# Optimization experiments

Measured on AMD Instinct MI355X. Metric: run time of the kernel, lower is better.

## Reference

```python
import jax, jax.numpy as jnp
import numpy as np


def setup_inputs() -> dict:
    key = jax.random.key(0)
    ks = jax.random.split(key, 8)
    T, S, W, O = 50000, 168, 336, 48
    N = T - W - O + 1
    x = jax.random.uniform(ks[0], (T,), minval=0.5, maxval=1.5, dtype=jnp.float32)
    noise = jax.random.normal(ks[1], (N, W), dtype=jnp.float32) * 0.001  # Normal(0, std=0.001)
    level_sc = jax.random.uniform(ks[2], (), minval=-1.0, maxval=1.0, dtype=jnp.float32)
    seas_sc = jax.random.uniform(ks[3], (), minval=-1.0, maxval=1.0, dtype=jnp.float32)
    init_seas = jax.random.uniform(ks[4], (S,), minval=0.65, maxval=1.35, dtype=jnp.float32)
    W1 = jax.random.normal(ks[5], (W, W), dtype=jnp.float32) / np.float32(np.sqrt(W))
    b1 = jnp.zeros((W,), jnp.float32)
    W2 = jax.random.normal(ks[6], (W, O), dtype=jnp.float32) / np.float32(np.sqrt(W))
    b2 = jnp.zeros((O,), jnp.float32)
    return {"x": x, "noise": noise, "level_sc": level_sc, "seas_sc": seas_sc,
            "init_seas": init_seas, "W1": W1, "b1": b1, "W2": W2, "b2": b2,
            "window_size": W, "out_size": O, "lvp": 1}


def reference(x, noise, level_sc, seas_sc, init_seas, W1, b1, W2, b2,
              window_size, out_size, lvp):
    T = x.shape[0]
    a = jax.nn.sigmoid(level_sc)      # level smoothing coeff
    g = jax.nn.sigmoid(seas_sc)       # seasonal smoothing coeff
    s0 = jnp.exp(init_seas)           # [S] initial multiplicative seasonals
    # seasonals list in torch: seas[0..S-1]=s0, seas[S]=s0[0], seas[S+i]=w_i.
    # Ring buffer holds seas[i..i+S-1] at step i (starting i=1): [s0[1:], s0[0]].
    buf0 = jnp.concatenate([s0[1:], s0[:1]])
    level0 = x[0] / s0[0]

    def step(carry, xi):
        level, buf = carry
        seas_i = buf[0]
        new_level = a * xi / seas_i + (1.0 - a) * level
        new_w = g * xi / new_level + (1.0 - g) * seas_i
        new_buf = jnp.concatenate([buf[1:], new_w[None]])
        return (new_level, new_buf), (new_level, new_w, jnp.log(new_level / level))

    _, (lvls, ws, logdiffs) = jax.lax.scan(step, (level0, buf0), x[1:])
    levels = jnp.concatenate([level0[None], lvls])        # [T]
    seas_full = jnp.concatenate([s0, s0[:1], ws])         # [S+T]

    d = logdiffs[1:] - logdiffs[:-1]
    level_var_loss = jnp.mean(d * d) * lvp

    N = T - window_size - out_size + 1
    idx_in = jnp.arange(N)[:, None] + jnp.arange(window_size)[None, :]   # [N,W]
    idx_lab = jnp.arange(N)[:, None] + window_size + jnp.arange(out_size)[None, :]  # [N,O]
    lev = levels[jnp.arange(N) + window_size][:, None]    # [N,1]
    inp = jnp.log(x[idx_in] / (lev * seas_full[idx_in])) + noise   # noisy squashed inputs
    labels = jnp.log(x[idx_lab] / (lev * seas_full[idx_lab]))

    h = jnp.tanh(inp @ W1 + b1)        # tanh_no_lstm: Linear(336,336)+tanh
    out = h @ W2 + b2                  # linear_no_lstm: Linear(336,48)
    return out, labels, level_var_loss
```

## Files before the change

kernel.cpp:

```cpp
#include <hip/hip_runtime.h>
#include <hip/hip_bf16.h>

typedef __attribute__((ext_vector_type(8))) short  s16x8;
typedef __attribute__((ext_vector_type(4))) short  s16x4;
typedef __attribute__((ext_vector_type(4))) float  f32x4;

#define T_LEN 50000
#define S_LEN 168
#define W_IN  336
#define O_OUT 48
#define N_ROWS (T_LEN - W_IN - O_OUT + 1)
#define N_PAD  49664
#define NBLK   (N_PAD / 64)

__device__ inline short f2bf(float f) {
    union { float f; unsigned u; } v; v.f = f;
    unsigned u = v.u;
    unsigned r = u + 0x7fffu + ((u >> 16) & 1u);
    return (short)(r >> 16);
}

__device__ inline int bfpk(float lo, float hi) {
    float2 f2; f2.x = lo; f2.y = hi;
    __hip_bfloat162 h = __float22bfloat162_rn(f2);
    int r; __builtin_memcpy(&r, &h, 4);
    return r;
}

__device__ inline float readlane_f(float v, int l) {
    return __int_as_float(__builtin_amdgcn_readlane(__float_as_int(v), l));
}

__device__ inline float fast_tanh(float v) {
    float e = __expf(2.f * v);
    return 1.f - 2.f * __builtin_amdgcn_rcpf(e + 1.f);
}

__global__ void k_preconvert(const float* __restrict__ W1, const float* __restrict__ W2,
                             short* __restrict__ W1T, short* __restrict__ W2T,
                             float* __restrict__ S1) {
    int idx = blockIdx.x * 256 + threadIdx.x;
    const int n1 = 352 * 352;
    const int n2 = n1 + 48 * 360;
    if (idx < n1) {
        int j = idx / 352, k = idx % 352;
        W1T[idx] = (j < 336 && k < 336) ? f2bf(W1[k * 336 + j]) : (short)0;
    } else if (idx < n2) {
        int i2 = idx - n1;
        int o = i2 / 360, k = i2 % 360;
        W2T[i2] = (k < 336) ? f2bf(W2[k * 48 + o]) : (short)0;
    } else if (idx < n2 + 352) {
        int j = idx - n2;
        float s = 0.f;
        if (j < 336)
            for (int k = 0; k < 336; ++k) s += W1[k * 336 + j];
        S1[j] = s;
    }
}

#define DPP_FMA(q_, CTRL, W, RM) { \
    int t_ = __builtin_amdgcn_update_dpp(0, __float_as_int(q_), (CTRL), (RM), 0xf, true); \
    q_ = fmaf((W), __int_as_float(t_), q_); }

__global__ void k_scan(const float* __restrict__ x, const float* __restrict__ level_sc,
                       const float* __restrict__ seas_sc, const float* __restrict__ init_seas,
                       float* __restrict__ lw, float* __restrict__ seasinit) {
    __shared__ float ring[256];
    int lane = threadIdx.x;
    float a = 1.f / (1.f + expf(-level_sc[0]));
    float g = 1.f / (1.f + expf(-seas_sc[0]));
    float om = 1.f - a, omg = 1.f - g;

    for (int t = lane; t < 256; t += 64) {
        float s = 1.f;
        if (t <= S_LEN) { s = expf(init_seas[t < S_LEN ? t : 0]); seasinit[t] = s; }
        ring[t] = s;
    }
    float lpv = x[0] / expf(init_seas[0]);
    if (lane == 0) { lw[0] = lpv; lw[1] = 1.f; }
    __syncthreads();

    float om1 = om, om2v = om1 * om1, om4 = om2v * om2v, om8 = om4 * om4;
    float pl    = powf(om, (float)(lane + 1));
    float fpre  = powf(om, (float)((lane & 15) + 1));
    float fpre2 = powf(om, (float)((lane & 31) + 1));

#define SCAN(QOUT, XV, RSV) { \
    float q_ = a * (XV) * (RSV); \
    DPP_FMA(q_, 0x111, om1,  0xf); \
    DPP_FMA(q_, 0x112, om2v, 0xf); \
    DPP_FMA(q_, 0x114, om4,  0xf); \
    DPP_FMA(q_, 0x118, om8,  0xf); \
    DPP_FMA(q_, 0x142, fpre,  0xa); \
    DPP_FMA(q_, 0x143, fpre2, 0xc); \
    QOUT = q_; }

#define XLOAD(I) float xr##I = x[1 + 64 * I + lane];
    XLOAD(0) XLOAD(1) XLOAD(2) XLOAD(3) XLOAD(4) XLOAD(5) XLOAD(6) XLOAD(7)
    XLOAD(8) XLOAD(9) XLOAD(10) XLOAD(11) XLOAD(12) XLOAD(13) XLOAD(14) XLOAD(15)
#undef XLOAD

    float sA0 = ring[1 + lane];
    float Qcur; SCAN(Qcur, xr0, __builtin_amdgcn_rcpf(sA0));
    float sW = sA0;
    float ldsA = ring[65 + lane];
    float ldsB;
    int ib = 1;

#define BODY(R, RN, LIN, LOUT, CLAMP) { \
    float lvl = fmaf(pl, lpv, Qcur); \
    lpv = readlane_f(lvl, 63); \
    float w_ = fmaf(omg, sW, (g * xr##R) * __builtin_amdgcn_rcpf(lvl)); \
    float2 pk_; pk_.x = lvl; pk_.y = w_; \
    *(float2*)&lw[2 * (ib + lane)] = pk_; \
    ring[(ib + S_LEN + lane) & 255] = w_; \
    LOUT = ring[(ib + 128 + lane) & 255]; \
    float Qn_; SCAN(Qn_, xr##RN, __builtin_amdgcn_rcpf(LIN)); \
    int pidx = ib + 1024 + lane; \
    if (CLAMP) pidx = pidx > (T_LEN - 1) ? (T_LEN - 1) : pidx; \
    xr##R = x[pidx]; \
    Qcur = Qn_; sW = LIN; \
    ib += 64; }

    for (int kb = 0; kb < 47; ++kb) {
        BODY(0,1,  ldsA, ldsB, 0) BODY(1,2,  ldsB, ldsA, 0) BODY(2,3,  ldsA, ldsB, 0) BODY(3,4,  ldsB, ldsA, 0)
        BODY(4,5,  ldsA, ldsB, 0) BODY(5,6,  ldsB, ldsA, 0) BODY(6,7,  ldsA, ldsB, 0) BODY(7,8,  ldsB, ldsA, 0)
        BODY(8,9,  ldsA, ldsB, 0) BODY(9,10, ldsB, ldsA, 0) BODY(10,11,ldsA, ldsB, 0) BODY(11,12,ldsB, ldsA, 0)
        BODY(12,13,ldsA, ldsB, 0) BODY(13,14,ldsB, ldsA, 0) BODY(14,15,ldsA, ldsB, 0) BODY(15,0, ldsB, ldsA, 0)
    }
    BODY(0,1,  ldsA, ldsB, 0) BODY(1,2,  ldsB, ldsA, 0) BODY(2,3,  ldsA, ldsB, 0) BODY(3,4,  ldsB, ldsA, 0)
    BODY(4,5,  ldsA, ldsB, 0) BODY(5,6,  ldsB, ldsA, 0) BODY(6,7,  ldsA, ldsB, 0) BODY(7,8,  ldsB, ldsA, 0)
    BODY(8,9,  ldsA, ldsB, 0) BODY(9,10, ldsB, ldsA, 0) BODY(10,11,ldsA, ldsB, 0) BODY(11,12,ldsB, ldsA, 0)
    BODY(12,13,ldsA, ldsB, 0)
    BODY(13,14,ldsB, ldsA, 1) BODY(14,15,ldsA, ldsB, 1) BODY(15,0, ldsB, ldsA, 1)
    BODY(0,1,  ldsA, ldsB, 1) BODY(1,2,  ldsB, ldsA, 1) BODY(2,3,  ldsA, ldsB, 1) BODY(3,4,  ldsB, ldsA, 1)
    BODY(4,5,  ldsA, ldsB, 1) BODY(5,6,  ldsB, ldsA, 1) BODY(6,7,  ldsA, ldsB, 1) BODY(7,8,  ldsB, ldsA, 1)
    BODY(8,9,  ldsA, ldsB, 1) BODY(9,10, ldsB, ldsA, 1) BODY(10,11,ldsA, ldsB, 1) BODY(11,12,ldsB, ldsA, 1)
#undef BODY

    {
        float lvl = fmaf(pl, lpv, Qcur);
        lpv = readlane_f(lvl, 63);
        float w_ = fmaf(omg, sW, (g * xr12) * __builtin_amdgcn_rcpf(lvl));
        float2 pk_; pk_.x = lvl; pk_.y = w_;
        *(float2*)&lw[2 * (49921 + lane)] = pk_;
    }
    {
        float Qn_; SCAN(Qn_, xr13, __builtin_amdgcn_rcpf(ldsA));
        float lvl = fmaf(pl, lpv, Qn_);
        if (lane < 15) {
            float w_ = fmaf(omg, ldsA, (g * xr13) * __builtin_amdgcn_rcpf(lvl));
            float2 pk_; pk_.x = lvl; pk_.y = w_;
            *(float2*)&lw[2 * (49985 + lane)] = pk_;
        }
    }
#undef SCAN
}

__global__ void k_logs(const float* __restrict__ x, const float* __restrict__ lw,
                       const float* __restrict__ seasinit,
                       float* __restrict__ F, float* __restrict__ llev,
                       float* __restrict__ partials) {
    __shared__ float sm[258];
    __shared__ float red[256];
    int tid = threadIdx.x;
    int t = blockIdx.x * 256 + tid;
    float ll = 0.f;
    if (t < T_LEN) {
        float2 cur = *(const float2*)&lw[2 * t];
        int ps = t - S_LEN; if (ps < 0) ps = 0;
        float sv = (t <= S_LEN) ? seasinit[t] : lw[2 * ps + 1];
        F[t]  = __logf(x[t]) - __logf(sv);
        ll    = __logf(cur.x);
        llev[t] = ll;
    }
    sm[tid] = ll;
    if (tid < 2) {
        int te = blockIdx.x * 256 + 256 + tid;
        sm[256 + tid] = (te < T_LEN) ? __logf(lw[2 * te]) : 0.f;
    }
    __syncthreads();
    float s = 0.f;
    if (t < T_LEN - 2) {
        float d = sm[tid + 2] - 2.f * sm[tid + 1] + sm[tid];
        s = d * d;
    }
    red[tid] = s; __syncthreads();
    for (int off = 128; off > 0; off >>= 1) {
        if (tid < off) red[tid] += red[tid + off];
        __syncthreads();
    }
    if (tid == 0) partials[blockIdx.x] = red[0];
}

__global__ __launch_bounds__(256, 3) void k_gemm(
        const float* __restrict__ noise, const float* __restrict__ F,
        const float* __restrict__ llev, const short* __restrict__ W1T,
        const float* __restrict__ b1, const short* __restrict__ W2T,
        const float* __restrict__ b2, const float* __restrict__ S1,
        const float* __restrict__ partials, const int* __restrict__ lvp,
        float* __restrict__ out, float* __restrict__ labels, float* __restrict__ loss) {
    __shared__ __align__(16) short hlds[64][360];
    __shared__ __align__(16) float Flds[448];
    __shared__ __align__(16) float Llds[64];
    __shared__ __align__(16) float b1lds[352];
    __shared__ __align__(16) float S1lds[352];

    int t = threadIdx.x, w = t >> 6, l = t & 63;
    int lm = l & 15, lq = l >> 4;
    long n0 = (long)blockIdx.x * 64;

    if (blockIdx.x == 0 && w == 3) {
        float s = partials[l] + partials[l + 64] + partials[l + 128];
        if (l < 4) s += partials[l + 192];
#pragma unroll
        for (int off = 32; off > 0; off >>= 1) s += __shfl_down(s, off, 64);
        if (l == 0) loss[0] = s / (float)(T_LEN - 2) * (float)lvp[0];
    }

    if (t < 112)      *(f32x4*)&Flds[t * 4] = *(const f32x4*)&F[n0 + t * 4];
    else if (t < 128) *(f32x4*)&Llds[(t - 112) * 4] = *(const f32x4*)&llev[n0 + W_IN + (t - 112) * 4];
    else if (t < 216) {
        int i4 = (t - 128) * 4;
        f32x4 v = (f32x4){0.f, 0.f, 0.f, 0.f};
        if (i4 < W_IN) v = *(const f32x4*)&b1[i4];
        *(f32x4*)&b1lds[i4] = v;
    } else if (t < 304 - 48) {
        int i4 = (t - 216) * 4;
        *(f32x4*)&S1lds[i4] = *(const f32x4*)&S1[i4];
    }
    if (t < 48) *(f32x4*)&S1lds[160 + t * 4] = *(const f32x4*)&S1[160 + t * 4];

    int rbase = (w >> 1) * 32;
    int jbase = (w & 1) * 176;
    long an0 = n0 + rbase + lm;      if (an0 > N_ROWS - 2) an0 = N_ROWS - 2;
    long an1 = n0 + rbase + 16 + lm; if (an1 > N_ROWS - 2) an1 = N_ROWS - 2;
    const float* nr0 = noise + an0 * W_IN + lq * 8;
    const float* nr1 = noise + an1 * W_IN + lq * 8;

    f32x4 nc00 = *(const f32x4*)&nr0[0], nc01 = *(const f32x4*)&nr0[4];
    f32x4 nc10 = *(const f32x4*)&nr1[0], nc11 = *(const f32x4*)&nr1[4];

    f32x4 acc0[11], acc1[11];
#pragma unroll
    for (int c = 0; c < 11; ++c) { acc0[c] = (f32x4){0,0,0,0}; acc1[c] = (f32x4){0,0,0,0}; }

    __syncthreads();

    const short* w1row = &W1T[(jbase + lm) * 352 + lq * 8];
#define LDW(CT, KS) (*(const s16x8*)&w1row[(CT) * 5632 + (KS) * 32])
#define MM2(CT, AF) \
    acc0[CT] = __builtin_amdgcn_mfma_f32_16x16x32_bf16(AF, bf0, acc0[CT], 0, 0, 0); \
    acc1[CT] = __builtin_amdgcn_mfma_f32_16x16x32_bf16(AF, bf1, acc1[CT], 0, 0, 0);

#define KSTEP(KS) { \
    s16x8 bf0, bf1; \
    { int fb = rbase + lm + (KS) * 32 + lq * 8; \
      int* b0i = (int*)&bf0; int* b1i = (int*)&bf1; \
      b0i[0] = bfpk(Flds[fb+0]  + nc00[0], Flds[fb+1]  + nc00[1]); \
      b0i[1] = bfpk(Flds[fb+2]  + nc00[2], Flds[fb+3]  + nc00[3]); \
      b0i[2] = bfpk(Flds[fb+4]  + nc01[0], Flds[fb+5]  + nc01[1]); \
      b0i[3] = bfpk(Flds[fb+6]  + nc01[2], Flds[fb+7]  + nc01[3]); \
      b1i[0] = bfpk(Flds[fb+16] + nc10[0], Flds[fb+17] + nc10[1]); \
      b1i[1] = bfpk(Flds[fb+18] + nc10[2], Flds[fb+19] + nc10[3]); \
      b1i[2] = bfpk(Flds[fb+20] + nc11[0], Flds[fb+21] + nc11[1]); \
      b1i[3] = bfpk(Flds[fb+22] + nc11[2], Flds[fb+23] + nc11[3]); } \
    if ((KS) < 10) { \
      nc00 = *(const f32x4*)&nr0[((KS)+1)*32]; nc01 = *(const f32x4*)&nr0[((KS)+1)*32+4]; \
      nc10 = *(const f32x4*)&nr1[((KS)+1)*32]; nc11 = *(const f32x4*)&nr1[((KS)+1)*32+4]; \
    } \
    s16x8 af0 = LDW(0,KS), af1 = LDW(1,KS), af2 = LDW(2,KS); \
    MM2(0, af0)  af0 = LDW(3,KS); \
    MM2(1, af1)  af1 = LDW(4,KS); \
    MM2(2, af2)  af2 = LDW(5,KS); \
    MM2(3, af0)  af0 = LDW(6,KS); \
    MM2(4, af1)  af1 = LDW(7,KS); \
    MM2(5, af2)  af2 = LDW(8,KS); \
    MM2(6, af0)  af0 = LDW(9,KS); \
    MM2(7, af1)  af1 = LDW(10,KS); \
    MM2(8, af2) \
    MM2(9, af0) \
    MM2(10, af1) \
}

    KSTEP(0) KSTEP(1) KSTEP(2) KSTEP(3) KSTEP(4) KSTEP(5)
    KSTEP(6) KSTEP(7) KSTEP(8) KSTEP(9) KSTEP(10)
#undef KSTEP
#undef MM2
#undef LDW

    float lv0 = Llds[rbase + lm], lv1 = Llds[rbase + 16 + lm];
#pragma unroll
    for (int ct = 0; ct < 11; ++ct) {
        f32x4 b1q = *(f32x4*)&b1lds[jbase + ct * 16 + lq * 4];
        f32x4 s1q = *(f32x4*)&S1lds[jbase + ct * 16 + lq * 4];
        int2 p0, p1;
        p0.x = bfpk(fast_tanh(fmaf(-lv0, s1q[0], acc0[ct][0] + b1q[0])),
                    fast_tanh(fmaf(-lv0, s1q[1], acc0[ct][1] + b1q[1])));
        p0.y = bfpk(fast_tanh(fmaf(-lv0, s1q[2], acc0[ct][2] + b1q[2])),
                    fast_tanh(fmaf(-lv0, s1q[3], acc0[ct][3] + b1q[3])));
        p1.x = bfpk(fast_tanh(fmaf(-lv1, s1q[0], acc1[ct][0] + b1q[0])),
                    fast_tanh(fmaf(-lv1, s1q[1], acc1[ct][1] + b1q[1])));
        p1.y = bfpk(fast_tanh(fmaf(-lv1, s1q[2], acc1[ct][2] + b1q[2])),
                    fast_tanh(fmaf(-lv1, s1q[3], acc1[ct][3] + b1q[3])));
        *(int2*)&hlds[rbase + lm][jbase + ct * 16 + lq * 4]      = p0;
        *(int2*)&hlds[rbase + 16 + lm][jbase + ct * 16 + lq * 4] = p1;
    }
    __syncthreads();

    f32x4 a2[3];
    a2[0] = (f32x4){0,0,0,0}; a2[1] = (f32x4){0,0,0,0}; a2[2] = (f32x4){0,0,0,0};
#pragma unroll
    for (int ks = 0; ks < 11; ++ks) {
        s16x8 hf = *(s16x8*)&hlds[w * 16 + lm][ks * 32 + lq * 8];
#pragma unroll
        for (int ct = 0; ct < 3; ++ct) {
            s16x8 bf2 = *(const s16x8*)&W2T[(ct * 16 + lm) * 360 + ks * 32 + lq * 8];
            a2[ct] = __builtin_amdgcn_mfma_f32_16x16x32_bf16(hf, bf2, a2[ct], 0, 0, 0);
        }
    }

    int rloc = w * 16 + lq * 4;
#pragma unroll
    for (int ct = 0; ct < 3; ++ct) {
        float b2v = b2[ct * 16 + lm];
#pragma unroll
        for (int r = 0; r < 4; ++r) {
            long row = n0 + rloc + r;
            if (row < N_ROWS) {
                int col = ct * 16 + lm;
                out[row * O_OUT + col]    = a2[ct][r] + b2v;
                labels[row * O_OUT + col] = Flds[rloc + r + W_IN + col] - Llds[rloc + r];
            }
        }
    }
}

extern "C" void kernel_launch(void* const* d_in, const int* in_sizes, int n_in,
                              void* d_out, int out_size, void* d_ws, size_t ws_size,
                              hipStream_t stream) {
    const float* x         = (const float*)d_in[0];
    const float* noise     = (const float*)d_in[1];
    const float* level_sc  = (const float*)d_in[2];
    const float* seas_sc   = (const float*)d_in[3];
    const float* init_seas = (const float*)d_in[4];
    const float* W1        = (const float*)d_in[5];
    const float* b1        = (const float*)d_in[6];
    const float* W2        = (const float*)d_in[7];
    const float* b2        = (const float*)d_in[8];
    const int*   lvp       = (const int*)d_in[11];

    float* out    = (float*)d_out;
    float* labels = out + (long)N_ROWS * O_OUT;
    float* loss   = labels + (long)N_ROWS * O_OUT;

    float* wsf      = (float*)d_ws;
    float* lw       = wsf;
    float* seasinit = wsf + 100096;
    float* F        = wsf + 100288;
    float* llev     = wsf + 150464;
    float* partials = wsf + 200512;
    float* S1f      = wsf + 200768;
    short* W1T      = (short*)(wsf + 201152);
    short* W2T      = W1T + 352 * 352;

    k_preconvert<<<554, 256, 0, stream>>>(W1, W2, W1T, W2T, S1f);
    k_scan<<<1, 64, 0, stream>>>(x, level_sc, seas_sc, init_seas, lw, seasinit);
    k_logs<<<196, 256, 0, stream>>>(x, lw, seasinit, F, llev, partials);
    k_gemm<<<NBLK, 256, 0, stream>>>(noise, F, llev, W1T, b1, W2T, b2, S1f,
                                     partials, lvp, out, labels, loss);
}
```

Measured before the change: 157.6 us.

## Split gemm block into eight waves with one row-tile each and offload labels

The first GEMM now runs on 512 threads per block: eight waves each own 16 rows instead of four waves owning 32, halving accumulator registers per wave and using double-buffered noise prefetch. In the second phase, waves 0-3 compute the output GEMM while waves 4-7 write labels in parallel. The aim is more waves in flight to hide latency and a shorter serial epilogue. In exchange, each W1 fragment loaded now feeds one MFMA instead of two, so W1 load traffic per MFMA doubles.

Result: slower. 175.2 us, median of 2 (+11.2%).

```diff
diff --git a/kernel.cpp b/kernel.cpp
--- a/kernel.cpp
+++ b/kernel.cpp
@@ -193,7 +193,7 @@
     if (tid == 0) partials[blockIdx.x] = red[0];
 }
 
-__global__ __launch_bounds__(256, 3) void k_gemm(
+__global__ __launch_bounds__(512, 2) void k_gemm(
         const float* __restrict__ noise, const float* __restrict__ F,
         const float* __restrict__ llev, const short* __restrict__ W1T,
         const float* __restrict__ b1, const short* __restrict__ W2T,
@@ -210,7 +210,7 @@
     int lm = l & 15, lq = l >> 4;
     long n0 = (long)blockIdx.x * 64;
 
-    if (blockIdx.x == 0 && w == 3) {
+    if (blockIdx.x == 0 && w == 7) {
         float s = partials[l] + partials[l + 64] + partials[l + 128];
         if (l < 4) s += partials[l + 192];
 #pragma unroll
@@ -225,113 +225,108 @@
         f32x4 v = (f32x4){0.f, 0.f, 0.f, 0.f};
         if (i4 < W_IN) v = *(const f32x4*)&b1[i4];
         *(f32x4*)&b1lds[i4] = v;
-    } else if (t < 304 - 48) {
+    } else if (t < 304) {
         int i4 = (t - 216) * 4;
         *(f32x4*)&S1lds[i4] = *(const f32x4*)&S1[i4];
     }
-    if (t < 48) *(f32x4*)&S1lds[160 + t * 4] = *(const f32x4*)&S1[160 + t * 4];
-
-    int rbase = (w >> 1) * 32;
+
+    int rbase = (w >> 1) * 16;
     int jbase = (w & 1) * 176;
-    long an0 = n0 + rbase + lm;      if (an0 > N_ROWS - 2) an0 = N_ROWS - 2;
-    long an1 = n0 + rbase + 16 + lm; if (an1 > N_ROWS - 2) an1 = N_ROWS - 2;
+    long an0 = n0 + rbase + lm; if (an0 > N_ROWS - 2) an0 = N_ROWS - 2;
     const float* nr0 = noise + an0 * W_IN + lq * 8;
-    const float* nr1 = noise + an1 * W_IN + lq * 8;
-
-    f32x4 nc00 = *(const f32x4*)&nr0[0], nc01 = *(const f32x4*)&nr0[4];
-    f32x4 nc10 = *(const f32x4*)&nr1[0], nc11 = *(const f32x4*)&nr1[4];
-
-    f32x4 acc0[11], acc1[11];
-#pragma unroll
-    for (int c = 0; c < 11; ++c) { acc0[c] = (f32x4){0,0,0,0}; acc1[c] = (f32x4){0,0,0,0}; }
+
+    f32x4 ncE0 = *(const f32x4*)&nr0[0],  ncE1 = *(const f32x4*)&nr0[4];
+    f32x4 ncO0 = *(const f32x4*)&nr0[32], ncO1 = *(const f32x4*)&nr0[36];
+
+    f32x4 acc[11];
+#pragma unroll
+    for (int c = 0; c < 11; ++c) acc[c] = (f32x4){0.f, 0.f, 0.f, 0.f};
 
     __syncthreads();
 
     const short* w1row = &W1T[(jbase + lm) * 352 + lq * 8];
 #define LDW(CT, KS) (*(const s16x8*)&w1row[(CT) * 5632 + (KS) * 32])
-#define MM2(CT, AF) \
-    acc0[CT] = __builtin_amdgcn_mfma_f32_16x16x32_bf16(AF, bf0, acc0[CT], 0, 0, 0); \
-    acc1[CT] = __builtin_amdgcn_mfma_f32_16x16x32_bf16(AF, bf1, acc1[CT], 0, 0, 0);
-
-#define KSTEP(KS) { \
-    s16x8 bf0, bf1; \
+#define MM(CT, AF) acc[CT] = __builtin_amdgcn_mfma_f32_16x16x32_bf16(AF, bf0, acc[CT], 0, 0, 0);
+
+#define KSTEP(KS, NC0, NC1) { \
+    s16x8 bf0; \
     { int fb = rbase + lm + (KS) * 32 + lq * 8; \
-      int* b0i = (int*)&bf0; int* b1i = (int*)&bf1; \
-      b0i[0] = bfpk(Flds[fb+0]  + nc00[0], Flds[fb+1]  + nc00[1]); \
-      b0i[1] = bfpk(Flds[fb+2]  + nc00[2], Flds[fb+3]  + nc00[3]); \
-      b0i[2] = bfpk(Flds[fb+4]  + nc01[0], Flds[fb+5]  + nc01[1]); \
-      b0i[3] = bfpk(Flds[fb+6]  + nc01[2], Flds[fb+7]  + nc01[3]); \
-      b1i[0] = bfpk(Flds[fb+16] + nc10[0], Flds[fb+17] + nc10[1]); \
-      b1i[1] = bfpk(Flds[fb+18] + nc10[2], Flds[fb+19] + nc10[3]); \
-      b1i[2] = bfpk(Flds[fb+20] + nc11[0], Flds[fb+21] + nc11[1]); \
-      b1i[3] = bfpk(Flds[fb+22] + nc11[2], Flds[fb+23] + nc11[3]); } \
-    if ((KS) < 10) { \
-      nc00 = *(const f32x4*)&nr0[((KS)+1)*32]; nc01 = *(const f32x4*)&nr0[((KS)+1)*32+4]; \
-      nc10 = *(const f32x4*)&nr1[((KS)+1)*32]; nc11 = *(const f32x4*)&nr1[((KS)+1)*32+4]; \
+      int* b0i = (int*)&bf0; \
+      b0i[0] = bfpk(Flds[fb+0] + NC0[0], Flds[fb+1] + NC0[1]); \
+      b0i[1] = bfpk(Flds[fb+2] + NC0[2], Flds[fb+3] + NC0[3]); \
+      b0i[2] = bfpk(Flds[fb+4] + NC1[0], Flds[fb+5] + NC1[1]); \
+      b0i[3] = bfpk(Flds[fb+6] + NC1[2], Flds[fb+7] + NC1[3]); } \
+    if ((KS) + 2 <= 10) { \
+      NC0 = *(const f32x4*)&nr0[((KS)+2)*32]; \
+      NC1 = *(const f32x4*)&nr0[((KS)+2)*32+4]; \
     } \
     s16x8 af0 = LDW(0,KS), af1 = LDW(1,KS), af2 = LDW(2,KS); \
-    MM2(0, af0)  af0 = LDW(3,KS); \
-    MM2(1, af1)  af1 = LDW(4,KS); \
-    MM2(2, af2)  af2 = LDW(5,KS); \
-    MM2(3, af0)  af0 = LDW(6,KS); \
-    MM2(4, af1)  af1 = LDW(7,KS); \
-    MM2(5, af2)  af2 = LDW(8,KS); \
-    MM2(6, af0)  af0 = LDW(9,KS); \
-    MM2(7, af1)  af1 = LDW(10,KS); \
-    MM2(8, af2) \
-    MM2(9, af0) \
-    MM2(10, af1) \
-}
-
-    KSTEP(0) KSTEP(1) KSTEP(2) KSTEP(3) KSTEP(4) KSTEP(5)
-    KSTEP(6) KSTEP(7) KSTEP(8) KSTEP(9) KSTEP(10)
+    MM(0, af0)  af0 = LDW(3,KS); \
+    MM(1, af1)  af1 = LDW(4,KS); \
+    MM(2, af2)  af2 = LDW(5,KS); \
+    MM(3, af0)  af0 = LDW(6,KS); \
+    MM(4, af1)  af1 = LDW(7,KS); \
+    MM(5, af2)  af2 = LDW(8,KS); \
+    MM(6, af0)  af0 = LDW(9,KS); \
+    MM(7, af1)  af1 = LDW(10,KS); \
+    MM(8, af2) \
+    MM(9, af0) \
+    MM(10, af1) \
+}
+
+    KSTEP(0, ncE0, ncE1) KSTEP(1, ncO0, ncO1) KSTEP(2, ncE0, ncE1) KSTEP(3, ncO0, ncO1)
+    KSTEP(4, ncE0, ncE1) KSTEP(5, ncO0, ncO1) KSTEP(6, ncE0, ncE1) KSTEP(7, ncO0, ncO1)
+    KSTEP(8, ncE0, ncE1) KSTEP(9, ncO0, ncO1) KSTEP(10, ncE0, ncE1)
 #undef KSTEP
-#undef MM2
+#undef MM
 #undef LDW
 
-    float lv0 = Llds[rbase + lm], lv1 = Llds[rbase + 16 + lm];
+    float lv0 = Llds[rbase + lm];
 #pragma unroll
     for (int ct = 0; ct < 11; ++ct) {
         f32x4 b1q = *(f32x4*)&b1lds[jbase + ct * 16 + lq * 4];
         f32x4 s1q = *(f32x4*)&S1lds[jbase + ct * 16 + lq * 4];
-        int2 p0, p1;
-        p0.x = bfpk(fast_tanh(fmaf(-lv0, s1q[0], acc0[ct][0] + b1q[0])),
-                    fast_tanh(fmaf(-lv0, s1q[1], acc0[ct][1] + b1q[1])));
-        p0.y = bfpk(fast_tanh(fmaf(-lv0, s1q[2], acc0[ct][2] + b1q[2])),
-                    fast_tanh(fmaf(-lv0, s1q[3], acc0[ct][3] + b1q[3])));
-        p1.x = bfpk(fast_tanh(fmaf(-lv1, s1q[0], acc1[ct][0] + b1q[0])),
-                    fast_tanh(fmaf(-lv1, s1q[1], acc1[ct][1] + b1q[1])));
-        p1.y = bfpk(fast_tanh(fmaf(-lv1, s1q[2], acc1[ct][2] + b1q[2])),
-                    fast_tanh(fmaf(-lv1, s1q[3], acc1[ct][3] + b1q[3])));
-        *(int2*)&hlds[rbase + lm][jbase + ct * 16 + lq * 4]      = p0;
-        *(int2*)&hlds[rbase + 16 + lm][jbase + ct * 16 + lq * 4] = p1;
+        int2 p0;
+        p0.x = bfpk(fast_tanh(fmaf(-lv0, s1q[0], acc[ct][0] + b1q[0])),
+                    fast_tanh(fmaf(-lv0, s1q[1], acc[ct][1] + b1q[1])));
+        p0.y = bfpk(fast_tanh(fmaf(-lv0, s1q[2], acc[ct][2] + b1q[2])),
+                    fast_tanh(fmaf(-lv0, s1q[3], acc[ct][3] + b1q[3])));
+        *(int2*)&hlds[rbase + lm][jbase + ct * 16 + lq * 4] = p0;
     }
     __syncthreads();
 
-    f32x4 a2[3];
-    a2[0] = (f32x4){0,0,0,0}; a2[1] = (f32x4){0,0,0,0}; a2[2] = (f32x4){0,0,0,0};
-#pragma unroll
-    for (int ks = 0; ks < 11; ++ks) {
-        s16x8 hf = *(s16x8*)&hlds[w * 16 + lm][ks * 32 + lq * 8];
+    if (w < 4) {
+        f32x4 a2[3];
+        a2[0] = (f32x4){0,0,0,0}; a2[1] = (f32x4){0,0,0,0}; a2[2] = (f32x4){0,0,0,0};
+#pragma unroll
+        for (int ks = 0; ks < 11; ++ks) {
+            s16x8 hf = *(s16x8*)&hlds[w * 16 + lm][ks * 32 + lq * 8];
+#pragma unroll
+            for (int ct = 0; ct < 3; ++ct) {
+                s16x8 bf2 = *(const s16x8*)&W2T[(ct * 16 + lm) * 360 + ks * 32 + lq * 8];
+                a2[ct] = __builtin_amdgcn_mfma_f32_16x16x32_bf16(hf, bf2, a2[ct], 0, 0, 0);
+            }
+        }
+        int rloc = w * 16 + lq * 4;
 #pragma unroll
         for (int ct = 0; ct < 3; ++ct) {
-            s16x8 bf2 = *(const s16x8*)&W2T[(ct * 16 + lm) * 360 + ks * 32 + lq * 8];
-            a2[ct] = __builtin_amdgcn_mfma_f32_16x16x32_bf16(hf, bf2, a2[ct], 0, 0, 0);
+            float b2v = b2[ct * 16 + lm];
+#pragma unroll
+            for (int r = 0; r < 4; ++r) {
+                long row = n0 + rloc + r;
+                if (row < N_ROWS) out[row * O_OUT + ct * 16 + lm] = a2[ct][r] + b2v;
+            }
         }
-    }
-
-    int rloc = w * 16 + lq * 4;
-#pragma unroll
-    for (int ct = 0; ct < 3; ++ct) {
-        float b2v = b2[ct * 16 + lm];
-#pragma unroll
-        for (int r = 0; r < 4; ++r) {
-            long row = n0 + rloc + r;
-            if (row < N_ROWS) {
-                int col = ct * 16 + lm;
-                out[row * O_OUT + col]    = a2[ct][r] + b2v;
-                labels[row * O_OUT + col] = Flds[rloc + r + W_IN + col] - Llds[rloc + r];
-            }
+    } else {
+        int rb2 = (w - 4) * 16;
+        int lrow = l >> 2, cbase = (l & 3) * 12;
+        long row = n0 + rb2 + lrow;
+        if (row < N_ROWS) {
+            float fl = -Llds[rb2 + lrow];
+            const float* fp = &Flds[rb2 + lrow + W_IN + cbase];
+            float* lp = &labels[row * O_OUT + cbase];
+#pragma unroll
+            for (int i = 0; i < 12; ++i) lp[i] = fp[i] + fl;
         }
     }
 }
@@ -367,6 +362,6 @@
     k_preconvert<<<554, 256, 0, stream>>>(W1, W2, W1T, W2T, S1f);
     k_scan<<<1, 64, 0, stream>>>(x, level_sc, seas_sc, init_seas, lw, seasinit);
     k_logs<<<196, 256, 0, stream>>>(x, lw, seasinit, F, llev, partials);
-    k_gemm<<<NBLK, 256, 0, stream>>>(noise, F, llev, W1T, b1, W2T, b2, S1f,
+    k_gemm<<<NBLK, 512, 0, stream>>>(noise, F, llev, W1T, b1, W2T, b2, S1f,
                                      partials, lvp, out, labels, loss);
 }
```
